# Optimization experiments

Measured on AMD Instinct MI355X. Metric: run time of the kernel, lower is better.

The kernel has to match this reference:

```python
import jax, jax.numpy as jnp
import numpy as np

VOCAB = 32000
D = 256        # embedding dim
NB = 256       # n_bubbles
NEQ = 5        # n_equilibrium_steps
THRESH = 1.5   # surprise_threshold
SEQ = 64
DECAYS = np.array([0.3, 0.7, 0.9], dtype=np.float32)  # RunningKnow frame decay rates


def setup_inputs() -> dict:
    key = jax.random.key(0)
    k1, k2, k3 = jax.random.split(key, 3)
    tokens = jax.random.randint(k1, (SEQ,), 0, VOCAB)
    E = jax.random.normal(k2, (VOCAB, D), dtype=jnp.float32)
    # Foam bubble measurement operators (stand-in: per-bubble linear map), scaled for sane stats
    W = jax.random.normal(k3, (NB, D, D), dtype=jnp.float32) / np.float32(np.sqrt(D))
    return {
        "tokens": tokens,
        "E": E,
        "W": W,
        "memory_decay_base": jnp.asarray(0.8, dtype=jnp.float32),
        "novelty_sensitivity": jnp.asarray(1.0, dtype=jnp.float32),
    }


def _equilibrate(m):
    # Stand-in for Foam.equilibrate: NEQ relaxation steps toward the bubble mean.
    for _ in range(NEQ):
        m = m + 0.1 * (m.mean(axis=0, keepdims=True) - m)
    return m


def reference(tokens, E, W, memory_decay_base, novelty_sensitivity):
    dr = jnp.asarray(DECAYS)[:, None, None]          # [F,1,1]
    F = dr.shape[0]
    sens = jnp.abs(novelty_sensitivity)

    def step(carry, tok):
        memory, means, vars_, n_seen = carry
        x = E[tok]                                   # [D]
        mm = memory.mean(axis=0)                     # [D]
        mem_norm = jnp.linalg.norm(mm) + 1e-10
        x_norm = jnp.linalg.norm(x) + 1e-10
        novelty = jnp.where(mem_norm > 1e-8,
                            1.0 - jnp.dot(x, mm) / (x_norm * mem_norm),
                            jnp.float32(1.0))
        decay = jax.nn.sigmoid(memory_decay_base - sens * novelty)
        xm = x + decay * mm                          # [D]

        meas = jnp.einsum('d,nde->ne', xm, W)        # [NB,D] bubble measurements

        # RunningKnow.evaluate (blank model at n_seen==0 -> never knows)
        std = jnp.sqrt(vars_ + 1e-8)                 # [F,NB,D]
        surprise = (jnp.abs(meas[None] - means) / std).mean(axis=(1, 2))  # [F]
        any_knows = jnp.any((surprise < THRESH) & (n_seen > 0))

        eq = _equilibrate(meas)
        eff = jnp.where(any_knows, meas, eq)         # know -> skip equilibration
        eff_d = jax.lax.stop_gradient(eff)           # .detach() in torch

        # RunningKnow.update (EMA mean/var per frame; first call initializes)
        upd_mean = dr * means + (1.0 - dr) * eff_d
        upd_var = jnp.maximum(dr * vars_ + (1.0 - dr) * (eff_d - means) * (eff_d - upd_mean), 1e-8)
        first = (n_seen == 0)
        means = jnp.where(first, jnp.broadcast_to(eff_d, (F, NB, D)), upd_mean)
        vars_ = jnp.where(first, jnp.float32(0.1), upd_var)

        # density matrix and spectrum
        mnorm = eff / (jnp.linalg.norm(eff, axis=-1, keepdims=True) + 1e-10)  # [NB,D]
        rho = mnorm.T @ mnorm / NB                   # [D,D]
        eigs = jnp.linalg.eigvalsh(jax.lax.stop_gradient(rho))
        eigs = jnp.maximum(eigs, 1e-12)
        eigs = eigs / eigs.sum()

        memory = decay * memory + (1.0 - decay) * eff_d
        logits = ((E @ rho) * E).sum(axis=-1)        # [VOCAB]
        return (memory, means, vars_, n_seen + 1), (logits, eigs)

    carry0 = (jnp.zeros((NB, D), jnp.float32),
              jnp.zeros((F, NB, D), jnp.float32),
              jnp.ones((F, NB, D), jnp.float32),
              jnp.int32(0))
    _, (logits, eigs) = jax.lax.scan(step, carry0, tokens)
    return logits, eigs  # [SEQ,VOCAB], [SEQ,D]
```

## Files before the change

kernel.cpp:

```cpp
#include <hip/hip_runtime.h>
#include <hip/hip_bf16.h>
#include <cstdint>
#include <cstddef>

constexpr size_t OFF_MEM    = 0;
constexpr size_t OFF_XM     = 65536;
constexpr size_t OFF_MU     = 82176;
constexpr size_t OFF_SABS   = 98560;
constexpr size_t OFF_BAR    = 98816;
constexpr size_t ZERO_END   = 98880;
constexpr size_t OFF_WBAR   = 98880;
constexpr size_t OFF_MEANS  = 164416;
constexpr size_t OFF_VARS   = 361024;
constexpr size_t OFF_DT     = 557632;
constexpr size_t OFF_ET     = 574016;
constexpr size_t OFF_RHO    = 590400;
constexpr size_t OFF_MN16   = 4784704;
constexpr size_t OFF_E16    = 6881856;
constexpr size_t WS_FLOATS  = 10977856;

#define SEQ_ 64
#define VOCAB_ 32000

typedef __attribute__((ext_vector_type(8))) short bf16x8;
typedef __attribute__((ext_vector_type(4))) float f32x4;

__device__ __forceinline__ float wave_sum(float v){
  v += __shfl_xor(v, 32); v += __shfl_xor(v, 16); v += __shfl_xor(v, 8);
  v += __shfl_xor(v, 4);  v += __shfl_xor(v, 2);  v += __shfl_xor(v, 1);
  return v;
}
__device__ __forceinline__ float block_sum(float v, float* red){
  int tid = threadIdx.x;
  v = wave_sum(v);
  if ((tid & 63) == 0) red[tid >> 6] = v;
  __syncthreads();
  float r = red[0] + red[1] + red[2] + red[3];
  __syncthreads();
  return r;
}
__device__ __forceinline__ float block_min(float v, float* red){
  int tid = threadIdx.x;
  v = fminf(v, __shfl_xor(v, 32)); v = fminf(v, __shfl_xor(v, 16));
  v = fminf(v, __shfl_xor(v, 8));  v = fminf(v, __shfl_xor(v, 4));
  v = fminf(v, __shfl_xor(v, 2));  v = fminf(v, __shfl_xor(v, 1));
  if ((tid & 63) == 0) red[tid >> 6] = v;
  __syncthreads();
  float r = fminf(fminf(red[0], red[1]), fminf(red[2], red[3]));
  __syncthreads();
  return r;
}
__device__ __forceinline__ float block_max(float v, float* red){
  int tid = threadIdx.x;
  v = fmaxf(v, __shfl_xor(v, 32)); v = fmaxf(v, __shfl_xor(v, 16));
  v = fmaxf(v, __shfl_xor(v, 8));  v = fmaxf(v, __shfl_xor(v, 4));
  v = fmaxf(v, __shfl_xor(v, 2));  v = fmaxf(v, __shfl_xor(v, 1));
  if ((tid & 63) == 0) red[tid >> 6] = v;
  __syncthreads();
  float r = fmaxf(fmaxf(red[0], red[1]), fmaxf(red[2], red[3]));
  __syncthreads();
  return r;
}

__global__ __launch_bounds__(256) void k0_init(const float* __restrict__ E, float* __restrict__ ws){
  size_t i = (size_t)blockIdx.x * 256 + threadIdx.x;
  if (i < ZERO_END) ws[i] = 0.f;
  __hip_bfloat16* e16 = (__hip_bfloat16*)(ws + OFF_E16);
  e16[i] = __float2bfloat16(E[i]);
}

__global__ __launch_bounds__(256) void k_wbar(const float* __restrict__ W, float* __restrict__ ws){
  size_t i = (size_t)blockIdx.x * 256 + threadIdx.x;
  float s = 0.f;
  #pragma unroll 4
  for (int n = 0; n < 256; ++n)
    s += W[(size_t)n * 65536 + i];
  ws[OFF_WBAR + i] = s * (1.0f / 256.0f);
}

__global__ __launch_bounds__(1024) void k_xm(const int* __restrict__ tokens,
    const float* __restrict__ E, const float* __restrict__ mdbp,
    const float* __restrict__ nsp, float* __restrict__ ws){
  __shared__ float xm_s[256];
  __shared__ __align__(16) float part[4][256];
  __shared__ float redA[16], redB[16], redC[16];
  const int tid = threadIdx.x;
  const int e = tid & 255, q = tid >> 8;
  const int lane = tid & 63, w = tid >> 6;
  const float sens = fabsf(nsp[0]);
  const float mdb  = mdbp[0];
  const float* Wb = ws + OFF_WBAR;
  float mm = 0.f;

  for (int t = 0; t < SEQ_; ++t){
    int tok = tokens[t];
    float xv = (tid < 256) ? E[(size_t)tok * 256 + e] : 0.f;
    float a = wave_sum(xv * mm);
    float b = wave_sum(xv * xv);
    float c = wave_sum(mm * mm);
    if (lane == 0){ redA[w] = a; redB[w] = b; redC[w] = c; }
    __syncthreads();
    float sdot = (redA[0] + redA[1]) + (redA[2] + redA[3]);
    float sx2  = (redB[0] + redB[1]) + (redB[2] + redB[3]);
    float sm2  = (redC[0] + redC[1]) + (redC[2] + redC[3]);
    float mem_norm = sqrtf(sm2) + 1e-10f;
    float x_norm   = sqrtf(sx2) + 1e-10f;
    float novelty = (mem_norm > 1e-8f) ? (1.0f - sdot / (x_norm * mem_norm)) : 1.0f;
    float z = mdb - sens * novelty;
    float decay = 1.0f / (1.0f + expf(-z));
    if (tid < 256){
      float xmv = xv + decay * mm;
      xm_s[e] = xmv;
      ws[OFF_XM + (size_t)e * 64 + t] = xmv;
    }
    __syncthreads();

    const float* Wq = Wb + (size_t)(q * 64) * 256 + e;
    float p = 0.f;
    #pragma unroll 16
    for (int dd = 0; dd < 64; ++dd)
      p = fmaf(xm_s[q * 64 + dd], Wq[(size_t)dd * 256], p);
    part[q][e] = p;
    __syncthreads();
    if (tid < 256){
      float acc = (part[0][e] + part[1][e]) + (part[2][e] + part[3][e]);
      ws[OFF_MU + (size_t)t * 256 + e] = acc;
      mm = decay * mm + (1.0f - decay) * acc;
    }
    __syncthreads();
  }
}

__global__ __launch_bounds__(256) void k_measall(const float* __restrict__ W, float* __restrict__ ws){
  __shared__ __align__(16) float xm_s[16384];
  const int tid = threadIdx.x, n = blockIdx.x;
  for (int i = tid; i < 16384; i += 256) xm_s[i] = ws[OFF_XM + i];
  __syncthreads();

  float acc[64];
  #pragma unroll
  for (int t = 0; t < 64; ++t) acc[t] = 0.f;

  const float* Wn = W + (size_t)n * 65536 + tid;
  for (int d = 0; d < 256; ++d){
    float wv = Wn[(size_t)d * 256];
    const float* xr = &xm_s[d * 64];
    #pragma unroll
    for (int q = 0; q < 16; ++q){
      float4 x4 = *(const float4*)&xr[q * 4];
      acc[q * 4 + 0] = fmaf(x4.x, wv, acc[q * 4 + 0]);
      acc[q * 4 + 1] = fmaf(x4.y, wv, acc[q * 4 + 1]);
      acc[q * 4 + 2] = fmaf(x4.z, wv, acc[q * 4 + 2]);
      acc[q * 4 + 3] = fmaf(x4.w, wv, acc[q * 4 + 3]);
    }
  }
  #pragma unroll
  for (int t = 0; t < 64; ++t)
    ws[OFF_RHO + (size_t)n * 16384 + (size_t)t * 256 + tid] = acc[t];
}

__global__ __launch_bounds__(1024, 1) void k_stats(float* __restrict__ ws){
  __shared__ float redA[16], redB[16], redC[16];
  const int tid = threadIdx.x;
  const int e = tid & 255, q = tid >> 8;
  const int lane = tid & 63, w = tid >> 6;
  const int n = blockIdx.x * 4 + q;
  unsigned* bar = (unsigned*)(ws + OFF_BAR);
  __hip_bfloat16* mn16 = (__hip_bfloat16*)(ws + OFF_MN16);
  const size_t ne = (size_t)n * 256 + e;
  const float TH = 1.5f * 65536.0f;
  const float c5 = 0.59049f;

  float mean0 = 0.f, mean1 = 0.f, mean2 = 0.f;
  float var0 = 0.f, var1 = 0.f, var2 = 0.f;

  for (int t = 0; t < SEQ_; ++t){
    float me = ws[OFF_RHO + (size_t)n * 16384 + (size_t)t * 256 + e];
    bool know = false;
    if (t > 0){
      float v0 = fabsf(me - mean0) / sqrtf(var0 + 1e-8f);
      float v1 = fabsf(me - mean1) / sqrtf(var1 + 1e-8f);
      float v2 = fabsf(me - mean2) / sqrtf(var2 + 1e-8f);
      float a = wave_sum(v0), b = wave_sum(v1), c = wave_sum(v2);
      if (lane == 0){ redA[w] = a; redB[w] = b; redC[w] = c; }
      __syncthreads();
      if (tid == 0){
        float sA = 0.f, sB = 0.f, sC = 0.f;
        #pragma unroll
        for (int i = 0; i < 16; ++i){ sA += redA[i]; sB += redB[i]; sC += redC[i]; }
        atomicAdd(&ws[OFF_SABS + (size_t)t * 4 + 0], sA);
        atomicAdd(&ws[OFF_SABS + (size_t)t * 4 + 1], sB);
        atomicAdd(&ws[OFF_SABS + (size_t)t * 4 + 2], sC);
        __hip_atomic_fetch_add(bar, 1u, __ATOMIC_ACQ_REL, __HIP_MEMORY_SCOPE_AGENT);
        unsigned tgt = 64u * (unsigned)t;
        while (__hip_atomic_load(bar, __ATOMIC_ACQUIRE, __HIP_MEMORY_SCOPE_AGENT) < tgt)
          __builtin_amdgcn_s_sleep(2);
      }
      __syncthreads();
      float s0 = __hip_atomic_load(&ws[OFF_SABS + (size_t)t * 4 + 0], __ATOMIC_RELAXED, __HIP_MEMORY_SCOPE_AGENT);
      float s1 = __hip_atomic_load(&ws[OFF_SABS + (size_t)t * 4 + 1], __ATOMIC_RELAXED, __HIP_MEMORY_SCOPE_AGENT);
      float s2 = __hip_atomic_load(&ws[OFF_SABS + (size_t)t * 4 + 2], __ATOMIC_RELAXED, __HIP_MEMORY_SCOPE_AGENT);
      know = (s0 < TH) || (s1 < TH) || (s2 < TH);
    }
    float mu = ws[OFF_MU + (size_t)t * 256 + e];
    float eq = c5 * me + (1.0f - c5) * mu;
    float eff = know ? me : eq;

    if (t == 0){
      mean0 = eff; mean1 = eff; mean2 = eff;
      var0 = 0.1f; var1 = 0.1f; var2 = 0.1f;
    } else {
      float um, uv;
      um = 0.3f * mean0 + 0.7f * eff;
      uv = 0.3f * var0 + 0.7f * (eff - mean0) * (eff - um);
      mean0 = um; var0 = fmaxf(uv, 1e-8f);
      um = 0.7f * mean1 + 0.3f * eff;
      uv = 0.7f * var1 + 0.3f * (eff - mean1) * (eff - um);
      mean1 = um; var1 = fmaxf(uv, 1e-8f);
      um = 0.9f * mean2 + 0.1f * eff;
      uv = 0.9f * var2 + 0.1f * (eff - mean2) * (eff - um);
      mean2 = um; var2 = fmaxf(uv, 1e-8f);
    }

    float nv = wave_sum(eff * eff);
    if (lane == 0) redA[w] = nv;
    __syncthreads();
    float nr2 = (redA[4 * q + 0] + redA[4 * q + 1]) + (redA[4 * q + 2] + redA[4 * q + 3]);
    float rn = sqrtf(nr2) + 1e-10f;
    mn16[(size_t)t * 65536 + ne] = __float2bfloat16(eff / rn);
    __syncthreads();
  }
}

__global__ __launch_bounds__(256) void k_rho(float* __restrict__ ws){
  const int t = blockIdx.x, rb = blockIdx.y, tid = threadIdx.x;
  __shared__ __align__(16) float tile[32][256];
  const __hip_bfloat16* mn16 = (const __hip_bfloat16*)(ws + OFF_MN16);
  float acc[32];
  #pragma unroll
  for (int i = 0; i < 32; ++i) acc[i] = 0.f;
  for (int c = 0; c < 8; ++c){
    __syncthreads();
    for (int j = tid; j < 8192; j += 256){
      int row = j >> 8, col = j & 255;
      tile[row][col] = __bfloat162float(mn16[(size_t)t * 65536 + (size_t)(c * 32 + row) * 256 + col]);
    }
    __syncthreads();
    for (int nl = 0; nl < 32; ++nl){
      float ev = tile[nl][tid];
      #pragma unroll
      for (int q = 0; q < 8; ++q){
        float4 dv = *(const float4*)&tile[nl][rb * 32 + q * 4];
        acc[q * 4 + 0] = fmaf(dv.x, ev, acc[q * 4 + 0]);
        acc[q * 4 + 1] = fmaf(dv.y, ev, acc[q * 4 + 1]);
        acc[q * 4 + 2] = fmaf(dv.z, ev, acc[q * 4 + 2]);
        acc[q * 4 + 3] = fmaf(dv.w, ev, acc[q * 4 + 3]);
      }
    }
  }
  #pragma unroll
  for (int i = 0; i < 32; ++i)
    ws[OFF_RHO + (size_t)t * 65536 + (size_t)(rb * 32 + i) * 256 + tid] = acc[i] * (1.0f / 256.0f);
}

__global__ __launch_bounds__(512, 2) void k_tri(float* __restrict__ ws){
  __shared__ __align__(16) float ca[256];
  __shared__ __align__(16) float ua[256];
  __shared__ __align__(16) float wa[256];
  __shared__ __align__(16) float ph[512];
  __shared__ float redA[8], redB[8];
  const int t = blockIdx.x, tid = threadIdx.x;
  const int c = tid & 255, h = tid >> 8;
  const float* rho = ws + OFF_RHO + (size_t)t * 65536;
  float* dT = ws + OFF_DT + (size_t)t * 256;
  float* eT = ws + OFF_ET + (size_t)t * 256;

  float Mreg[128];
  {
    const float* Mc = rho + (size_t)(h * 128) * 256 + c;
    #pragma unroll
    for (int rr = 0; rr < 128; ++rr)
      Mreg[rr] = Mc[(size_t)rr * 256];
  }
  const int rowbase = h * 128;

  for (int k = 0; k < 254; ++k){
    __syncthreads();
    if (c == k){
      #pragma unroll
      for (int rr = 0; rr < 128; ++rr) ca[rowbase + rr] = Mreg[rr];
    }
    __syncthreads();
    float uval = 0.f;
    if (tid < 256){
      float raw = ca[tid];
      uval = (tid > k) ? raw : 0.f;
      ua[tid] = uval;
      if (tid == 0) dT[k] = ca[k];
    }
    float pa = wave_sum(uval * uval);
    if ((tid & 63) == 0) redA[tid >> 6] = pa;
    __syncthreads();
    float sigma2 = redA[0] + redA[1] + redA[2] + redA[3]
                 + redA[4] + redA[5] + redA[6] + redA[7];
    float v0 = ca[k + 1];
    if (sigma2 < 1e-30f){
      if (tid == 0) eT[k] = v0;
      continue;
    }
    float sig = sqrtf(sigma2);
    float alpha = (v0 >= 0.f) ? -sig : sig;
    float u0 = v0 - alpha;
    float beta = 2.0f / (sigma2 - v0 * v0 + u0 * u0);
    if (tid == 0) eT[k] = alpha;
    if (tid == k + 1) ua[tid] = u0;
    __syncthreads();

    {
      float a0 = 0.f, a1 = 0.f, a2 = 0.f, a3 = 0.f;
      #pragma unroll
      for (int rr = 0; rr < 128; rr += 4){
        float4 u4 = *(const float4*)&ua[rowbase + rr];
        a0 = fmaf(Mreg[rr + 0], u4.x, a0);
        a1 = fmaf(Mreg[rr + 1], u4.y, a1);
        a2 = fmaf(Mreg[rr + 2], u4.z, a2);
        a3 = fmaf(Mreg[rr + 3], u4.w, a3);
      }
      ph[tid] = (a0 + a1) + (a2 + a3);
    }
    __syncthreads();
    float p = ph[c] + ph[c + 256];
    float up = (tid < 256) ? ua[tid] * p : 0.f;
    float pb = wave_sum(up);
    if ((tid & 63) == 0) redB[tid >> 6] = pb;
    __syncthreads();
    float s = redB[0] + redB[1] + redB[2] + redB[3]
            + redB[4] + redB[5] + redB[6] + redB[7];
    if (tid < 256) wa[tid] = (tid > k) ? (beta * p - 0.5f * beta * beta * s * ua[tid]) : 0.f;
    __syncthreads();
    {
      float ucv = ua[c], wcv = wa[c];
      #pragma unroll
      for (int rr = 0; rr < 128; rr += 4){
        float4 u4 = *(const float4*)&ua[rowbase + rr];
        float4 w4 = *(const float4*)&wa[rowbase + rr];
        Mreg[rr + 0] = fmaf(-w4.x, ucv, fmaf(-u4.x, wcv, Mreg[rr + 0]));
        Mreg[rr + 1] = fmaf(-w4.y, ucv, fmaf(-u4.y, wcv, Mreg[rr + 1]));
        Mreg[rr + 2] = fmaf(-w4.z, ucv, fmaf(-u4.z, wcv, Mreg[rr + 2]));
        Mreg[rr + 3] = fmaf(-w4.w, ucv, fmaf(-u4.w, wcv, Mreg[rr + 3]));
      }
    }
  }

  __syncthreads();
  if (c == 254){
    #pragma unroll
    for (int rr = 0; rr < 128; ++rr) ca[rowbase + rr] = Mreg[rr];
  }
  __syncthreads();
  if (tid == 0){ dT[254] = ca[254]; eT[254] = ca[255]; }
  __syncthreads();
  if (c == 255){
    #pragma unroll
    for (int rr = 0; rr < 128; ++rr) ca[rowbase + rr] = Mreg[rr];
  }
  __syncthreads();
  if (tid == 0){ dT[255] = ca[255]; eT[255] = 0.f; }
}

__global__ __launch_bounds__(256) void k_bisect(const float* __restrict__ ws, float* __restrict__ out){
  __shared__ float d_s[256];
  __shared__ float e2_s[256];
  __shared__ float ea_s[256];
  __shared__ float red[4];
  const int t = blockIdx.x, tid = threadIdx.x;
  d_s[tid] = ws[OFF_DT + (size_t)t * 256 + tid];
  float evv = (tid < 255) ? ws[OFF_ET + (size_t)t * 256 + tid] : 0.f;
  e2_s[tid] = evv * evv;
  ea_s[tid] = fabsf(evv);
  __syncthreads();
  float rad = ea_s[tid] + ((tid > 0) ? ea_s[tid - 1] : 0.f);
  float glo = block_min(d_s[tid] - rad, red);
  float ghi = block_max(d_s[tid] + rad, red);

  float l = glo, h = ghi;
  for (int it = 0; it < 40; ++it){
    float mid = 0.5f * (l + h);
    float q = d_s[0] - mid;
    int cnt = (q < 0.f) ? 1 : 0;
    #pragma unroll 8
    for (int i = 1; i < 256; ++i){
      float qr = __builtin_amdgcn_rcpf(q);
      q = (d_s[i] - mid) - e2_s[i - 1] * qr;
      q = (fabsf(q) < 1e-25f) ? -1e-25f : q;
      cnt += (q < 0.f) ? 1 : 0;
    }
    if (cnt <= tid) l = mid; else h = mid;
  }
  float lam = fmaxf(0.5f * (l + h), 1e-12f);
  float ssum = block_sum(lam, red);
  out[(size_t)SEQ_ * VOCAB_ + (size_t)t * 256 + tid] = lam / ssum;
}

__global__ __launch_bounds__(512) void k_gemm(const float* __restrict__ ws, float* __restrict__ out){
  __shared__ __align__(16) short A_lds[128 * 64];
  __shared__ __align__(16) short B_lds[256 * 64];
  __shared__ float pl[8][64];
  const int tid = threadIdx.x;
  const int bx = blockIdx.x, t = blockIdx.y;
  const int lane = tid & 63, w = tid >> 6;
  const int wr = w >> 2, wc = w & 3;
  const int vbase = bx * 128;
  const short* E16 = (const short*)(ws + OFF_E16);
  const short* MN  = (const short*)(ws + OFF_MN16) + (size_t)t * 65536;

  f32x4 acc[4][4];
  #pragma unroll
  for (int i = 0; i < 4; ++i)
    #pragma unroll
    for (int j = 0; j < 4; ++j){ f32x4 z = {0.f, 0.f, 0.f, 0.f}; acc[i][j] = z; }

  const int g = lane >> 4, r16 = lane & 15;
  const int sx = r16 & 7;
  for (int it = 0; it < 4; ++it){
    const int k0 = it * 64;
    __syncthreads();
    #pragma unroll
    for (int pa = 0; pa < 2; ++pa){
      int ch = pa * 512 + tid;
      int row = ch >> 3, c8 = ch & 7;
      int sc8 = c8 ^ (row & 7);
      uint4 v = *(const uint4*)(E16 + (size_t)(vbase + row) * 256 + k0 + sc8 * 8);
      *(uint4*)&A_lds[ch * 8] = v;
    }
    #pragma unroll
    for (int pb = 0; pb < 4; ++pb){
      int ch = pb * 512 + tid;
      int row = ch >> 3, c8 = ch & 7;
      int sc8 = c8 ^ (row & 7);
      uint4 v = *(const uint4*)(MN + (size_t)row * 256 + k0 + sc8 * 8);
      *(uint4*)&B_lds[ch * 8] = v;
    }
    __syncthreads();
    #pragma unroll
    for (int kk = 0; kk < 64; kk += 32){
      const int j0 = (kk >> 3) + g;
      bf16x8 af[4], bf[4];
      #pragma unroll
      for (int fm = 0; fm < 4; ++fm)
        af[fm] = *(const bf16x8*)&A_lds[(wr * 64 + fm * 16 + r16) * 64 + (j0 ^ sx) * 8];
      #pragma unroll
      for (int fn = 0; fn < 4; ++fn)
        bf[fn] = *(const bf16x8*)&B_lds[(wc * 64 + fn * 16 + r16) * 64 + (j0 ^ sx) * 8];
      #pragma unroll
      for (int fm = 0; fm < 4; ++fm)
        #pragma unroll
        for (int fn = 0; fn < 4; ++fn)
          acc[fm][fn] = __builtin_amdgcn_mfma_f32_16x16x32_bf16(af[fm], bf[fn], acc[fm][fn], 0, 0, 0);
    }
  }

  float ps[4][4];
  #pragma unroll
  for (int fm = 0; fm < 4; ++fm)
    #pragma unroll
    for (int i = 0; i < 4; ++i){
      float sv = 0.f;
      #pragma unroll
      for (int fn = 0; fn < 4; ++fn){ float v = acc[fm][fn][i]; sv += v * v; }
      sv += __shfl_xor(sv, 1); sv += __shfl_xor(sv, 2);
      sv += __shfl_xor(sv, 4); sv += __shfl_xor(sv, 8);
      ps[fm][i] = sv;
    }
  __syncthreads();
  if (r16 == 0){
    #pragma unroll
    for (int fm = 0; fm < 4; ++fm)
      #pragma unroll
      for (int i = 0; i < 4; ++i)
        pl[w][fm * 16 + g * 4 + i] = ps[fm][i];
  }
  __syncthreads();
  if (tid < 128){
    int rr = tid;
    int wrr = rr >> 6, lr = rr & 63;
    float sum = pl[wrr * 4 + 0][lr] + pl[wrr * 4 + 1][lr] + pl[wrr * 4 + 2][lr] + pl[wrr * 4 + 3][lr];
    out[(size_t)t * VOCAB_ + vbase + rr] = sum * (1.0f / 256.0f);
  }
}

extern "C" void kernel_launch(void* const* d_in, const int* in_sizes, int n_in,
                              void* d_out, int out_size, void* d_ws, size_t ws_size,
                              hipStream_t stream){
  const int*   tokens = (const int*)d_in[0];
  const float* E      = (const float*)d_in[1];
  const float* W      = (const float*)d_in[2];
  const float* mdbp   = (const float*)d_in[3];
  const float* nsp    = (const float*)d_in[4];
  float* out = (float*)d_out;
  float* ws  = (float*)d_ws;
  if (ws_size < WS_FLOATS * sizeof(float)) return;

  k0_init<<<dim3(32000), dim3(256), 0, stream>>>(E, ws);
  k_wbar<<<dim3(256), dim3(256), 0, stream>>>(W, ws);
  k_xm<<<dim3(1), dim3(1024), 0, stream>>>(tokens, E, mdbp, nsp, ws);
  k_measall<<<dim3(256), dim3(256), 0, stream>>>(W, ws);
  {
    void* args[1];
    args[0] = (void*)&ws;
    hipLaunchCooperativeKernel((const void*)k_stats, dim3(64), dim3(1024), args, 0, stream);
  }
  k_rho<<<dim3(64, 8), dim3(256), 0, stream>>>(ws);
  k_tri<<<dim3(64), dim3(512), 0, stream>>>(ws);
  k_bisect<<<dim3(64), dim3(256), 0, stream>>>(ws, out);
  k_gemm<<<dim3(250, 64), dim3(512), 0, stream>>>(ws, out);
}
```

Before: 3.537 ms.

## Fuse bisection into tridiagonalization kernel and cut per-step barriers

Each Householder step in k_tri now has fewer barriers. The next pivot column is written to shared memory at the end of the previous iteration instead of getting its own barrier pair. The w-vector is recomputed inline from the partial products, which removes a shared array and a barrier, and the u·p dot product is taken directly from the per-half partials. The eigenvalue bisection now runs inside the same kernel on d/e values kept in shared memory, which removes a kernel launch and the global round-trip of the tridiagonal. In exchange, bisection runs duplicated across both 256-thread halves, and only one half writes the results.

```diff
diff --git a/kernel.cpp b/kernel.cpp
--- a/kernel.cpp
+++ b/kernel.cpp
@@ -36,28 +36,6 @@
   if ((tid & 63) == 0) red[tid >> 6] = v;
   __syncthreads();
   float r = red[0] + red[1] + red[2] + red[3];
-  __syncthreads();
-  return r;
-}
-__device__ __forceinline__ float block_min(float v, float* red){
-  int tid = threadIdx.x;
-  v = fminf(v, __shfl_xor(v, 32)); v = fminf(v, __shfl_xor(v, 16));
-  v = fminf(v, __shfl_xor(v, 8));  v = fminf(v, __shfl_xor(v, 4));
-  v = fminf(v, __shfl_xor(v, 2));  v = fminf(v, __shfl_xor(v, 1));
-  if ((tid & 63) == 0) red[tid >> 6] = v;
-  __syncthreads();
-  float r = fminf(fminf(red[0], red[1]), fminf(red[2], red[3]));
-  __syncthreads();
-  return r;
-}
-__device__ __forceinline__ float block_max(float v, float* red){
-  int tid = threadIdx.x;
-  v = fmaxf(v, __shfl_xor(v, 32)); v = fmaxf(v, __shfl_xor(v, 16));
-  v = fmaxf(v, __shfl_xor(v, 8));  v = fmaxf(v, __shfl_xor(v, 4));
-  v = fmaxf(v, __shfl_xor(v, 2));  v = fmaxf(v, __shfl_xor(v, 1));
-  if ((tid & 63) == 0) red[tid >> 6] = v;
-  __syncthreads();
-  float r = fmaxf(fmaxf(red[0], red[1]), fmaxf(red[2], red[3]));
   __syncthreads();
   return r;
 }
@@ -263,17 +241,17 @@
     ws[OFF_RHO + (size_t)t * 65536 + (size_t)(rb * 32 + i) * 256 + tid] = acc[i] * (1.0f / 256.0f);
 }
 
-__global__ __launch_bounds__(512, 2) void k_tri(float* __restrict__ ws){
+__global__ __launch_bounds__(512, 2) void k_tri(float* __restrict__ ws, float* __restrict__ out){
   __shared__ __align__(16) float ca[256];
   __shared__ __align__(16) float ua[256];
-  __shared__ __align__(16) float wa[256];
+  __shared__ __align__(16) float dd[256];
+  __shared__ __align__(16) float ee[256];
   __shared__ __align__(16) float ph[512];
   __shared__ float redA[8], redB[8];
   const int t = blockIdx.x, tid = threadIdx.x;
   const int c = tid & 255, h = tid >> 8;
+  const int lane = tid & 63, w = tid >> 6;
   const float* rho = ws + OFF_RHO + (size_t)t * 65536;
-  float* dT = ws + OFF_DT + (size_t)t * 256;
-  float* eT = ws + OFF_ET + (size_t)t * 256;
 
   float Mreg[128];
   {
@@ -284,122 +262,138 @@
   }
   const int rowbase = h * 128;
 
+  if (c == 0){
+    #pragma unroll
+    for (int rr = 0; rr < 128; ++rr) ca[rowbase + rr] = Mreg[rr];
+  }
+  __syncthreads();
+
   for (int k = 0; k < 254; ++k){
-    __syncthreads();
-    if (c == k){
-      #pragma unroll
-      for (int rr = 0; rr < 128; ++rr) ca[rowbase + rr] = Mreg[rr];
-    }
-    __syncthreads();
     float uval = 0.f;
     if (tid < 256){
       float raw = ca[tid];
       uval = (tid > k) ? raw : 0.f;
       ua[tid] = uval;
-      if (tid == 0) dT[k] = ca[k];
+      if (tid == 0) dd[k] = ca[k];
     }
     float pa = wave_sum(uval * uval);
-    if ((tid & 63) == 0) redA[tid >> 6] = pa;
+    if (lane == 0) redA[w] = pa;
     __syncthreads();
     float sigma2 = redA[0] + redA[1] + redA[2] + redA[3]
                  + redA[4] + redA[5] + redA[6] + redA[7];
     float v0 = ca[k + 1];
     if (sigma2 < 1e-30f){
-      if (tid == 0) eT[k] = v0;
+      if (tid == 0) ee[k] = v0;
+      __syncthreads();
+      if (c == k + 1){
+        #pragma unroll
+        for (int rr = 0; rr < 128; ++rr) ca[rowbase + rr] = Mreg[rr];
+      }
+      __syncthreads();
       continue;
     }
     float sig = sqrtf(sigma2);
     float alpha = (v0 >= 0.f) ? -sig : sig;
     float u0 = v0 - alpha;
     float beta = 2.0f / (sigma2 - v0 * v0 + u0 * u0);
-    if (tid == 0) eT[k] = alpha;
+    if (tid == 0) ee[k] = alpha;
     if (tid == k + 1) ua[tid] = u0;
     __syncthreads();
 
-    {
-      float a0 = 0.f, a1 = 0.f, a2 = 0.f, a3 = 0.f;
-      #pragma unroll
-      for (int rr = 0; rr < 128; rr += 4){
-        float4 u4 = *(const float4*)&ua[rowbase + rr];
-        a0 = fmaf(Mreg[rr + 0], u4.x, a0);
-        a1 = fmaf(Mreg[rr + 1], u4.y, a1);
-        a2 = fmaf(Mreg[rr + 2], u4.z, a2);
-        a3 = fmaf(Mreg[rr + 3], u4.w, a3);
-      }
-      ph[tid] = (a0 + a1) + (a2 + a3);
-    }
-    __syncthreads();
-    float p = ph[c] + ph[c + 256];
-    float up = (tid < 256) ? ua[tid] * p : 0.f;
-    float pb = wave_sum(up);
-    if ((tid & 63) == 0) redB[tid >> 6] = pb;
+    float a0 = 0.f, a1 = 0.f, a2 = 0.f, a3 = 0.f;
+    #pragma unroll
+    for (int rr = 0; rr < 128; rr += 4){
+      float4 u4 = *(const float4*)&ua[rowbase + rr];
+      a0 = fmaf(Mreg[rr + 0], u4.x, a0);
+      a1 = fmaf(Mreg[rr + 1], u4.y, a1);
+      a2 = fmaf(Mreg[rr + 2], u4.z, a2);
+      a3 = fmaf(Mreg[rr + 3], u4.w, a3);
+    }
+    float partial = (a0 + a1) + (a2 + a3);
+    float pmask = (c > k) ? partial : 0.f;
+    ph[tid] = pmask;
+    float ucv = ua[c];
+    float ssp = wave_sum(ucv * pmask);
+    if (lane == 0) redB[w] = ssp;
     __syncthreads();
     float s = redB[0] + redB[1] + redB[2] + redB[3]
             + redB[4] + redB[5] + redB[6] + redB[7];
-    if (tid < 256) wa[tid] = (tid > k) ? (beta * p - 0.5f * beta * beta * s * ua[tid]) : 0.f;
-    __syncthreads();
-    {
-      float ucv = ua[c], wcv = wa[c];
-      #pragma unroll
-      for (int rr = 0; rr < 128; rr += 4){
-        float4 u4 = *(const float4*)&ua[rowbase + rr];
-        float4 w4 = *(const float4*)&wa[rowbase + rr];
-        Mreg[rr + 0] = fmaf(-w4.x, ucv, fmaf(-u4.x, wcv, Mreg[rr + 0]));
-        Mreg[rr + 1] = fmaf(-w4.y, ucv, fmaf(-u4.y, wcv, Mreg[rr + 1]));
-        Mreg[rr + 2] = fmaf(-w4.z, ucv, fmaf(-u4.z, wcv, Mreg[rr + 2]));
-        Mreg[rr + 3] = fmaf(-w4.w, ucv, fmaf(-u4.w, wcv, Mreg[rr + 3]));
-      }
-    }
-  }
-
-  __syncthreads();
-  if (c == 254){
-    #pragma unroll
-    for (int rr = 0; rr < 128; ++rr) ca[rowbase + rr] = Mreg[rr];
-  }
-  __syncthreads();
-  if (tid == 0){ dT[254] = ca[254]; eT[254] = ca[255]; }
-  __syncthreads();
-  if (c == 255){
-    #pragma unroll
-    for (int rr = 0; rr < 128; ++rr) ca[rowbase + rr] = Mreg[rr];
-  }
-  __syncthreads();
-  if (tid == 0){ dT[255] = ca[255]; eT[255] = 0.f; }
-}
-
-__global__ __launch_bounds__(256) void k_bisect(const float* __restrict__ ws, float* __restrict__ out){
-  __shared__ float d_s[256];
-  __shared__ float e2_s[256];
-  __shared__ float ea_s[256];
-  __shared__ float red[4];
-  const int t = blockIdx.x, tid = threadIdx.x;
-  d_s[tid] = ws[OFF_DT + (size_t)t * 256 + tid];
-  float evv = (tid < 255) ? ws[OFF_ET + (size_t)t * 256 + tid] : 0.f;
-  e2_s[tid] = evv * evv;
-  ea_s[tid] = fabsf(evv);
-  __syncthreads();
-  float rad = ea_s[tid] + ((tid > 0) ? ea_s[tid - 1] : 0.f);
-  float glo = block_min(d_s[tid] - rad, red);
-  float ghi = block_max(d_s[tid] + rad, red);
-
-  float l = glo, h = ghi;
+    float gamma = 0.5f * beta * beta * s;
+    float pc = ph[c] + ph[c + 256];
+    float wcv = fmaf(-gamma, ucv, beta * pc);
+
+    #pragma unroll
+    for (int rr = 0; rr < 128; rr += 4){
+      float4 u4 = *(const float4*)&ua[rowbase + rr];
+      float4 pA = *(const float4*)&ph[rowbase + rr];
+      float4 pB = *(const float4*)&ph[rowbase + rr + 256];
+      float w0 = fmaf(-gamma, u4.x, beta * (pA.x + pB.x));
+      float w1 = fmaf(-gamma, u4.y, beta * (pA.y + pB.y));
+      float w2 = fmaf(-gamma, u4.z, beta * (pA.z + pB.z));
+      float w3 = fmaf(-gamma, u4.w, beta * (pA.w + pB.w));
+      Mreg[rr + 0] = fmaf(-w0, ucv, fmaf(-u4.x, wcv, Mreg[rr + 0]));
+      Mreg[rr + 1] = fmaf(-w1, ucv, fmaf(-u4.y, wcv, Mreg[rr + 1]));
+      Mreg[rr + 2] = fmaf(-w2, ucv, fmaf(-u4.z, wcv, Mreg[rr + 2]));
+      Mreg[rr + 3] = fmaf(-w3, ucv, fmaf(-u4.w, wcv, Mreg[rr + 3]));
+    }
+    if (c == k + 1){
+      #pragma unroll
+      for (int rr = 0; rr < 128; ++rr) ca[rowbase + rr] = Mreg[rr];
+    }
+    __syncthreads();
+  }
+
+  if (tid == 511) ua[0] = Mreg[127];
+  __syncthreads();
+  if (tid == 0){
+    dd[254] = ca[254];  ee[254] = ca[255];
+    dd[255] = ua[0];    ee[255] = 0.f;
+  }
+  __syncthreads();
+
+  float dvv = dd[c];
+  float evv = ee[c];
+  if (h == 0){ ua[c] = evv * evv; ph[c] = fabsf(evv); }
+  __syncthreads();
+  float rad = ph[c] + ((c > 0) ? ph[c - 1] : 0.f);
+  float vmin = dvv - rad, vmax = dvv + rad;
+  vmin = fminf(vmin, __shfl_xor(vmin, 32)); vmin = fminf(vmin, __shfl_xor(vmin, 16));
+  vmin = fminf(vmin, __shfl_xor(vmin, 8));  vmin = fminf(vmin, __shfl_xor(vmin, 4));
+  vmin = fminf(vmin, __shfl_xor(vmin, 2));  vmin = fminf(vmin, __shfl_xor(vmin, 1));
+  vmax = fmaxf(vmax, __shfl_xor(vmax, 32)); vmax = fmaxf(vmax, __shfl_xor(vmax, 16));
+  vmax = fmaxf(vmax, __shfl_xor(vmax, 8));  vmax = fmaxf(vmax, __shfl_xor(vmax, 4));
+  vmax = fmaxf(vmax, __shfl_xor(vmax, 2));  vmax = fmaxf(vmax, __shfl_xor(vmax, 1));
+  if (lane == 0){ redA[w] = vmin; redB[w] = vmax; }
+  __syncthreads();
+  float glo = fminf(fminf(fminf(redA[0], redA[1]), fminf(redA[2], redA[3])),
+                    fminf(fminf(redA[4], redA[5]), fminf(redA[6], redA[7])));
+  float ghi = fmaxf(fmaxf(fmaxf(redB[0], redB[1]), fmaxf(redB[2], redB[3])),
+                    fmaxf(fmaxf(redB[4], redB[5]), fmaxf(redB[6], redB[7])));
+  __syncthreads();
+
+  float lo = glo, hi = ghi;
   for (int it = 0; it < 40; ++it){
-    float mid = 0.5f * (l + h);
-    float q = d_s[0] - mid;
+    float mid = 0.5f * (lo + hi);
+    float q = dd[0] - mid;
     int cnt = (q < 0.f) ? 1 : 0;
     #pragma unroll 8
     for (int i = 1; i < 256; ++i){
       float qr = __builtin_amdgcn_rcpf(q);
-      q = (d_s[i] - mid) - e2_s[i - 1] * qr;
+      q = (dd[i] - mid) - ua[i - 1] * qr;
       q = (fabsf(q) < 1e-25f) ? -1e-25f : q;
       cnt += (q < 0.f) ? 1 : 0;
     }
-    if (cnt <= tid) l = mid; else h = mid;
-  }
-  float lam = fmaxf(0.5f * (l + h), 1e-12f);
-  float ssum = block_sum(lam, red);
-  out[(size_t)SEQ_ * VOCAB_ + (size_t)t * 256 + tid] = lam / ssum;
+    if (cnt <= c) lo = mid; else hi = mid;
+  }
+  float lam = fmaxf(0.5f * (lo + hi), 1e-12f);
+  float lp = (h == 0) ? lam : 0.f;
+  lp = wave_sum(lp);
+  if (lane == 0) redA[w] = lp;
+  __syncthreads();
+  float ssum = ((redA[0] + redA[1]) + (redA[2] + redA[3]))
+             + ((redA[4] + redA[5]) + (redA[6] + redA[7]));
+  if (h == 0)
+    out[(size_t)SEQ_ * VOCAB_ + (size_t)t * 256 + c] = lam / ssum;
 }
 
 __global__ __launch_bounds__(512) void k_gemm(const float* __restrict__ ws, float* __restrict__ out){
@@ -511,7 +505,6 @@
     hipLaunchCooperativeKernel((const void*)k_stats, dim3(64), dim3(1024), args, 0, stream);
   }
   k_rho<<<dim3(64, 8), dim3(256), 0, stream>>>(ws);
-  k_tri<<<dim3(64), dim3(512), 0, stream>>>(ws);
-  k_bisect<<<dim3(64), dim3(256), 0, stream>>>(ws, out);
+  k_tri<<<dim3(64), dim3(512), 0, stream>>>(ws, out);
   k_gemm<<<dim3(250, 64), dim3(512), 0, stream>>>(ws, out);
 }
```

Result: slower. 3.805 ms (+7.6%).

## Merge tridiagonalization and logits GEMM into one launch so they overlap

Applied to the files above, without the earlier changes.

Combines the serial Householder tridiagonalization (64 blocks) and the independent bf16 MFMA logits GEMM into a single kernel, with the block index choosing the role. The 64 latency-bound tri blocks can then run alongside the many GEMM blocks instead of leaving most of the GPU idle. The GEMM code is unchanged apart from using shared memory carved from a common buffer. In exchange, the merged kernel inherits the tri path's register pressure and launch bounds, which may reduce GEMM occupancy.

```diff
diff --git a/kernel.cpp b/kernel.cpp
--- a/kernel.cpp
+++ b/kernel.cpp
@@ -263,109 +263,201 @@
     ws[OFF_RHO + (size_t)t * 65536 + (size_t)(rb * 32 + i) * 256 + tid] = acc[i] * (1.0f / 256.0f);
 }
 
-__global__ __launch_bounds__(512, 2) void k_tri(float* __restrict__ ws){
-  __shared__ __align__(16) float ca[256];
-  __shared__ __align__(16) float ua[256];
-  __shared__ __align__(16) float wa[256];
-  __shared__ __align__(16) float ph[512];
-  __shared__ float redA[8], redB[8];
-  const int t = blockIdx.x, tid = threadIdx.x;
-  const int c = tid & 255, h = tid >> 8;
-  const float* rho = ws + OFF_RHO + (size_t)t * 65536;
-  float* dT = ws + OFF_DT + (size_t)t * 256;
-  float* eT = ws + OFF_ET + (size_t)t * 256;
-
-  float Mreg[128];
-  {
-    const float* Mc = rho + (size_t)(h * 128) * 256 + c;
+__global__ __launch_bounds__(512, 2) void k_trigemm(float* __restrict__ ws, float* __restrict__ out){
+  __shared__ __align__(16) char smem_raw[51200];
+  const int tid = threadIdx.x;
+
+  if (blockIdx.x < 64){
+    float* ca   = (float*)smem_raw;
+    float* ua   = ca + 256;
+    float* wa   = ua + 256;
+    float* ph   = wa + 256;
+    float* redA = ph + 512;
+    float* redB = redA + 8;
+    const int t = blockIdx.x;
+    const int c = tid & 255, h = tid >> 8;
+    const float* rho = ws + OFF_RHO + (size_t)t * 65536;
+    float* dT = ws + OFF_DT + (size_t)t * 256;
+    float* eT = ws + OFF_ET + (size_t)t * 256;
+
+    float Mreg[128];
+    {
+      const float* Mc = rho + (size_t)(h * 128) * 256 + c;
+      #pragma unroll
+      for (int rr = 0; rr < 128; ++rr)
+        Mreg[rr] = Mc[(size_t)rr * 256];
+    }
+    const int rowbase = h * 128;
+
+    for (int k = 0; k < 254; ++k){
+      __syncthreads();
+      if (c == k){
+        #pragma unroll
+        for (int rr = 0; rr < 128; ++rr) ca[rowbase + rr] = Mreg[rr];
+      }
+      __syncthreads();
+      float uval = 0.f;
+      if (tid < 256){
+        float raw = ca[tid];
+        uval = (tid > k) ? raw : 0.f;
+        ua[tid] = uval;
+        if (tid == 0) dT[k] = ca[k];
+      }
+      float pa = wave_sum(uval * uval);
+      if ((tid & 63) == 0) redA[tid >> 6] = pa;
+      __syncthreads();
+      float sigma2 = redA[0] + redA[1] + redA[2] + redA[3]
+                   + redA[4] + redA[5] + redA[6] + redA[7];
+      float v0 = ca[k + 1];
+      if (sigma2 < 1e-30f){
+        if (tid == 0) eT[k] = v0;
+        continue;
+      }
+      float sig = sqrtf(sigma2);
+      float alpha = (v0 >= 0.f) ? -sig : sig;
+      float u0 = v0 - alpha;
+      float beta = 2.0f / (sigma2 - v0 * v0 + u0 * u0);
+      if (tid == 0) eT[k] = alpha;
+      if (tid == k + 1) ua[tid] = u0;
+      __syncthreads();
+
+      {
+        float a0 = 0.f, a1 = 0.f, a2 = 0.f, a3 = 0.f;
+        #pragma unroll
+        for (int rr = 0; rr < 128; rr += 4){
+          float4 u4 = *(const float4*)&ua[rowbase + rr];
+          a0 = fmaf(Mreg[rr + 0], u4.x, a0);
+          a1 = fmaf(Mreg[rr + 1], u4.y, a1);
+          a2 = fmaf(Mreg[rr + 2], u4.z, a2);
+          a3 = fmaf(Mreg[rr + 3], u4.w, a3);
+        }
+        ph[tid] = (a0 + a1) + (a2 + a3);
+      }
+      __syncthreads();
+      float p = ph[c] + ph[c + 256];
+      float up = (tid < 256) ? ua[tid] * p : 0.f;
+      float pb = wave_sum(up);
+      if ((tid & 63) == 0) redB[tid >> 6] = pb;
+      __syncthreads();
+      float s = redB[0] + redB[1] + redB[2] + redB[3]
+              + redB[4] + redB[5] + redB[6] + redB[7];
+      if (tid < 256) wa[tid] = (tid > k) ? (beta * p - 0.5f * beta * beta * s * ua[tid]) : 0.f;
+      __syncthreads();
+      {
+        float ucv = ua[c], wcv = wa[c];
+        #pragma unroll
+        for (int rr = 0; rr < 128; rr += 4){
+          float4 u4 = *(const float4*)&ua[rowbase + rr];
+          float4 w4 = *(const float4*)&wa[rowbase + rr];
+          Mreg[rr + 0] = fmaf(-w4.x, ucv, fmaf(-u4.x, wcv, Mreg[rr + 0]));
+          Mreg[rr + 1] = fmaf(-w4.y, ucv, fmaf(-u4.y, wcv, Mreg[rr + 1]));
+          Mreg[rr + 2] = fmaf(-w4.z, ucv, fmaf(-u4.z, wcv, Mreg[rr + 2]));
+          Mreg[rr + 3] = fmaf(-w4.w, ucv, fmaf(-u4.w, wcv, Mreg[rr + 3]));
+        }
+      }
+    }
+
+    __syncthreads();
+    if (c == 254){
+      #pragma unroll
+      for (int rr = 0; rr < 128; ++rr) ca[rowbase + rr] = Mreg[rr];
+    }
+    __syncthreads();
+    if (tid == 0){ dT[254] = ca[254]; eT[254] = ca[255]; }
+    __syncthreads();
+    if (c == 255){
+      #pragma unroll
+      for (int rr = 0; rr < 128; ++rr) ca[rowbase + rr] = Mreg[rr];
+    }
+    __syncthreads();
+    if (tid == 0){ dT[255] = ca[255]; eT[255] = 0.f; }
+  } else {
+    short* A_lds = (short*)smem_raw;
+    short* B_lds = A_lds + 8192;
+    float* pl    = (float*)(B_lds + 16384);
+    const int g = blockIdx.x - 64;
+    const int bx = g % 250, t = g / 250;
+    const int lane = tid & 63, w = tid >> 6;
+    const int wr = w >> 2, wc = w & 3;
+    const int vbase = bx * 128;
+    const short* E16 = (const short*)(ws + OFF_E16);
+    const short* MN  = (const short*)(ws + OFF_MN16) + (size_t)t * 65536;
+
+    f32x4 acc[4][4];
     #pragma unroll
-    for (int rr = 0; rr < 128; ++rr)
-      Mreg[rr] = Mc[(size_t)rr * 256];
-  }
-  const int rowbase = h * 128;
-
-  for (int k = 0; k < 254; ++k){
-    __syncthreads();
-    if (c == k){
-      #pragma unroll
-      for (int rr = 0; rr < 128; ++rr) ca[rowbase + rr] = Mreg[rr];
-    }
-    __syncthreads();
-    float uval = 0.f;
-    if (tid < 256){
-      float raw = ca[tid];
-      uval = (tid > k) ? raw : 0.f;
-      ua[tid] = uval;
-      if (tid == 0) dT[k] = ca[k];
-    }
-    float pa = wave_sum(uval * uval);
-    if ((tid & 63) == 0) redA[tid >> 6] = pa;
-    __syncthreads();
-    float sigma2 = redA[0] + redA[1] + redA[2] + redA[3]
-                 + redA[4] + redA[5] + redA[6] + redA[7];
-    float v0 = ca[k + 1];
-    if (sigma2 < 1e-30f){
-      if (tid == 0) eT[k] = v0;
-      continue;
-    }
-    float sig = sqrtf(sigma2);
-    float alpha = (v0 >= 0.f) ? -sig : sig;
-    float u0 = v0 - alpha;
-    float beta = 2.0f / (sigma2 - v0 * v0 + u0 * u0);
-    if (tid == 0) eT[k] = alpha;
-    if (tid == k + 1) ua[tid] = u0;
-    __syncthreads();
-
-    {
-      float a0 = 0.f, a1 = 0.f, a2 = 0.f, a3 = 0.f;
-      #pragma unroll
-      for (int rr = 0; rr < 128; rr += 4){
-        float4 u4 = *(const float4*)&ua[rowbase + rr];
-        a0 = fmaf(Mreg[rr + 0], u4.x, a0);
-        a1 = fmaf(Mreg[rr + 1], u4.y, a1);
-        a2 = fmaf(Mreg[rr + 2], u4.z, a2);
-        a3 = fmaf(Mreg[rr + 3], u4.w, a3);
-      }
-      ph[tid] = (a0 + a1) + (a2 + a3);
-    }
-    __syncthreads();
-    float p = ph[c] + ph[c + 256];
-    float up = (tid < 256) ? ua[tid] * p : 0.f;
-    float pb = wave_sum(up);
-    if ((tid & 63) == 0) redB[tid >> 6] = pb;
-    __syncthreads();
-    float s = redB[0] + redB[1] + redB[2] + redB[3]
-            + redB[4] + redB[5] + redB[6] + redB[7];
-    if (tid < 256) wa[tid] = (tid > k) ? (beta * p - 0.5f * beta * beta * s * ua[tid]) : 0.f;
-    __syncthreads();
-    {
-      float ucv = ua[c], wcv = wa[c];
-      #pragma unroll
-      for (int rr = 0; rr < 128; rr += 4){
-        float4 u4 = *(const float4*)&ua[rowbase + rr];
-        float4 w4 = *(const float4*)&wa[rowbase + rr];
-        Mreg[rr + 0] = fmaf(-w4.x, ucv, fmaf(-u4.x, wcv, Mreg[rr + 0]));
-        Mreg[rr + 1] = fmaf(-w4.y, ucv, fmaf(-u4.y, wcv, Mreg[rr + 1]));
-        Mreg[rr + 2] = fmaf(-w4.z, ucv, fmaf(-u4.z, wcv, Mreg[rr + 2]));
-        Mreg[rr + 3] = fmaf(-w4.w, ucv, fmaf(-u4.w, wcv, Mreg[rr + 3]));
-      }
-    }
-  }
-
-  __syncthreads();
-  if (c == 254){
+    for (int i = 0; i < 4; ++i)
+      #pragma unroll
+      for (int j = 0; j < 4; ++j){ f32x4 z = {0.f, 0.f, 0.f, 0.f}; acc[i][j] = z; }
+
+    const int gq = lane >> 4, r16 = lane & 15;
+    const int sx = r16 & 7;
+    for (int it = 0; it < 4; ++it){
+      const int k0 = it * 64;
+      __syncthreads();
+      #pragma unroll
+      for (int pa = 0; pa < 2; ++pa){
+        int ch = pa * 512 + tid;
+        int row = ch >> 3, c8 = ch & 7;
+        int sc8 = c8 ^ (row & 7);
+        uint4 v = *(const uint4*)(E16 + (size_t)(vbase + row) * 256 + k0 + sc8 * 8);
+        *(uint4*)&A_lds[ch * 8] = v;
+      }
+      #pragma unroll
+      for (int pb = 0; pb < 4; ++pb){
+        int ch = pb * 512 + tid;
+        int row = ch >> 3, c8 = ch & 7;
+        int sc8 = c8 ^ (row & 7);
+        uint4 v = *(const uint4*)(MN + (size_t)row * 256 + k0 + sc8 * 8);
+        *(uint4*)&B_lds[ch * 8] = v;
+      }
+      __syncthreads();
+      #pragma unroll
+      for (int kk = 0; kk < 64; kk += 32){
+        const int j0 = (kk >> 3) + gq;
+        bf16x8 af[4], bf[4];
+        #pragma unroll
+        for (int fm = 0; fm < 4; ++fm)
+          af[fm] = *(const bf16x8*)&A_lds[(wr * 64 + fm * 16 + r16) * 64 + (j0 ^ sx) * 8];
+        #pragma unroll
+        for (int fn = 0; fn < 4; ++fn)
+          bf[fn] = *(const bf16x8*)&B_lds[(wc * 64 + fn * 16 + r16) * 64 + (j0 ^ sx) * 8];
+        #pragma unroll
+        for (int fm = 0; fm < 4; ++fm)
+          #pragma unroll
+          for (int fn = 0; fn < 4; ++fn)
+            acc[fm][fn] = __builtin_amdgcn_mfma_f32_16x16x32_bf16(af[fm], bf[fn], acc[fm][fn], 0, 0, 0);
+      }
+    }
+
+    float ps[4][4];
     #pragma unroll
-    for (int rr = 0; rr < 128; ++rr) ca[rowbase + rr] = Mreg[rr];
-  }
-  __syncthreads();
-  if (tid == 0){ dT[254] = ca[254]; eT[254] = ca[255]; }
-  __syncthreads();
-  if (c == 255){
-    #pragma unroll
-    for (int rr = 0; rr < 128; ++rr) ca[rowbase + rr] = Mreg[rr];
-  }
-  __syncthreads();
-  if (tid == 0){ dT[255] = ca[255]; eT[255] = 0.f; }
+    for (int fm = 0; fm < 4; ++fm)
+      #pragma unroll
+      for (int i = 0; i < 4; ++i){
+        float sv = 0.f;
+        #pragma unroll
+        for (int fn = 0; fn < 4; ++fn){ float v = acc[fm][fn][i]; sv += v * v; }
+        sv += __shfl_xor(sv, 1); sv += __shfl_xor(sv, 2);
+        sv += __shfl_xor(sv, 4); sv += __shfl_xor(sv, 8);
+        ps[fm][i] = sv;
+      }
+    __syncthreads();
+    if (r16 == 0){
+      #pragma unroll
+      for (int fm = 0; fm < 4; ++fm)
+        #pragma unroll
+        for (int i = 0; i < 4; ++i)
+          pl[w * 64 + fm * 16 + gq * 4 + i] = ps[fm][i];
+    }
+    __syncthreads();
+    if (tid < 128){
+      int rr = tid;
+      int wrr = rr >> 6, lr = rr & 63;
+      float sum = pl[(wrr * 4 + 0) * 64 + lr] + pl[(wrr * 4 + 1) * 64 + lr]
+                + pl[(wrr * 4 + 2) * 64 + lr] + pl[(wrr * 4 + 3) * 64 + lr];
+      out[(size_t)t * VOCAB_ + vbase + rr] = sum * (1.0f / 256.0f);
+    }
+  }
 }
 
 __global__ __launch_bounds__(256) void k_bisect(const float* __restrict__ ws, float* __restrict__ out){
@@ -402,93 +494,6 @@
   out[(size_t)SEQ_ * VOCAB_ + (size_t)t * 256 + tid] = lam / ssum;
 }
 
-__global__ __launch_bounds__(512) void k_gemm(const float* __restrict__ ws, float* __restrict__ out){
-  __shared__ __align__(16) short A_lds[128 * 64];
-  __shared__ __align__(16) short B_lds[256 * 64];
-  __shared__ float pl[8][64];
-  const int tid = threadIdx.x;
-  const int bx = blockIdx.x, t = blockIdx.y;
-  const int lane = tid & 63, w = tid >> 6;
-  const int wr = w >> 2, wc = w & 3;
-  const int vbase = bx * 128;
-  const short* E16 = (const short*)(ws + OFF_E16);
-  const short* MN  = (const short*)(ws + OFF_MN16) + (size_t)t * 65536;
-
-  f32x4 acc[4][4];
-  #pragma unroll
-  for (int i = 0; i < 4; ++i)
-    #pragma unroll
-    for (int j = 0; j < 4; ++j){ f32x4 z = {0.f, 0.f, 0.f, 0.f}; acc[i][j] = z; }
-
-  const int g = lane >> 4, r16 = lane & 15;
-  const int sx = r16 & 7;
-  for (int it = 0; it < 4; ++it){
-    const int k0 = it * 64;
-    __syncthreads();
-    #pragma unroll
-    for (int pa = 0; pa < 2; ++pa){
-      int ch = pa * 512 + tid;
-      int row = ch >> 3, c8 = ch & 7;
-      int sc8 = c8 ^ (row & 7);
-      uint4 v = *(const uint4*)(E16 + (size_t)(vbase + row) * 256 + k0 + sc8 * 8);
-      *(uint4*)&A_lds[ch * 8] = v;
-    }
-    #pragma unroll
-    for (int pb = 0; pb < 4; ++pb){
-      int ch = pb * 512 + tid;
-      int row = ch >> 3, c8 = ch & 7;
-      int sc8 = c8 ^ (row & 7);
-      uint4 v = *(const uint4*)(MN + (size_t)row * 256 + k0 + sc8 * 8);
-      *(uint4*)&B_lds[ch * 8] = v;
-    }
-    __syncthreads();
-    #pragma unroll
-    for (int kk = 0; kk < 64; kk += 32){
-      const int j0 = (kk >> 3) + g;
-      bf16x8 af[4], bf[4];
-      #pragma unroll
-      for (int fm = 0; fm < 4; ++fm)
-        af[fm] = *(const bf16x8*)&A_lds[(wr * 64 + fm * 16 + r16) * 64 + (j0 ^ sx) * 8];
-      #pragma unroll
-      for (int fn = 0; fn < 4; ++fn)
-        bf[fn] = *(const bf16x8*)&B_lds[(wc * 64 + fn * 16 + r16) * 64 + (j0 ^ sx) * 8];
-      #pragma unroll
-      for (int fm = 0; fm < 4; ++fm)
-        #pragma unroll
-        for (int fn = 0; fn < 4; ++fn)
-          acc[fm][fn] = __builtin_amdgcn_mfma_f32_16x16x32_bf16(af[fm], bf[fn], acc[fm][fn], 0, 0, 0);
-    }
-  }
-
-  float ps[4][4];
-  #pragma unroll
-  for (int fm = 0; fm < 4; ++fm)
-    #pragma unroll
-    for (int i = 0; i < 4; ++i){
-      float sv = 0.f;
-      #pragma unroll
-      for (int fn = 0; fn < 4; ++fn){ float v = acc[fm][fn][i]; sv += v * v; }
-      sv += __shfl_xor(sv, 1); sv += __shfl_xor(sv, 2);
-      sv += __shfl_xor(sv, 4); sv += __shfl_xor(sv, 8);
-      ps[fm][i] = sv;
-    }
-  __syncthreads();
-  if (r16 == 0){
-    #pragma unroll
-    for (int fm = 0; fm < 4; ++fm)
-      #pragma unroll
-      for (int i = 0; i < 4; ++i)
-        pl[w][fm * 16 + g * 4 + i] = ps[fm][i];
-  }
-  __syncthreads();
-  if (tid < 128){
-    int rr = tid;
-    int wrr = rr >> 6, lr = rr & 63;
-    float sum = pl[wrr * 4 + 0][lr] + pl[wrr * 4 + 1][lr] + pl[wrr * 4 + 2][lr] + pl[wrr * 4 + 3][lr];
-    out[(size_t)t * VOCAB_ + vbase + rr] = sum * (1.0f / 256.0f);
-  }
-}
-
 extern "C" void kernel_launch(void* const* d_in, const int* in_sizes, int n_in,
                               void* d_out, int out_size, void* d_ws, size_t ws_size,
                               hipStream_t stream){
@@ -511,7 +516,6 @@
     hipLaunchCooperativeKernel((const void*)k_stats, dim3(64), dim3(1024), args, 0, stream);
   }
   k_rho<<<dim3(64, 8), dim3(256), 0, stream>>>(ws);
-  k_tri<<<dim3(64), dim3(512), 0, stream>>>(ws);
+  k_trigemm<<<dim3(64 + 250 * 64), dim3(512), 0, stream>>>(ws, out);
   k_bisect<<<dim3(64), dim3(256), 0, stream>>>(ws, out);
-  k_gemm<<<dim3(250, 64), dim3(512), 0, stream>>>(ws, out);
-}
+}
```

New measurement: 3.182 ms. 10.0% less time.
